# Optimization experiments

Hardware: AMD Instinct MI355X
Metric: run time of the kernel (lower is better)

The kernel has to match this reference:

```python
import jax, jax.numpy as jnp
import numpy as np

D_MODEL = 1024
N_HEADS = 16
HEAD_DIM = D_MODEL // N_HEADS
MAX_LEN = 32768
Q_LEN = 16
START_POS = MAX_LEN - Q_LEN
SCALE = 1.0 / np.sqrt(HEAD_DIM)


def setup_inputs() -> dict:
    key = jax.random.key(0)
    ks = jax.random.split(key, 7)
    xav = np.sqrt(6.0 / (D_MODEL + D_MODEL))  # xavier_uniform bound
    return {
        "query": jax.random.normal(ks[0], (Q_LEN, D_MODEL), dtype=jnp.float32),
        "Wq": jax.random.uniform(ks[1], (D_MODEL, D_MODEL), jnp.float32, -xav, xav),
        "Wk": jax.random.uniform(ks[2], (D_MODEL, D_MODEL), jnp.float32, -xav, xav),
        "Wv": jax.random.uniform(ks[3], (D_MODEL, D_MODEL), jnp.float32, -xav, xav),
        "Wo": jax.random.uniform(ks[4], (D_MODEL, D_MODEL), jnp.float32, -xav, xav),
        "cache_k": jax.random.normal(ks[5], (MAX_LEN, N_HEADS, HEAD_DIM), dtype=jnp.float32),
        "cache_v": jax.random.normal(ks[6], (MAX_LEN, N_HEADS, HEAD_DIM), dtype=jnp.float32),
        "start_pos": START_POS,
    }


def reference(query, Wq, Wk, Wv, Wo, cache_k, cache_v, start_pos):
    S = query.shape[0]
    # QKV projections (nn.Linear: y = x @ W.T), reshape to [S, H, hd]
    Q = (query @ Wq.T).reshape(S, N_HEADS, HEAD_DIM)
    K = (query @ Wk.T).reshape(S, N_HEADS, HEAD_DIM)
    V = (query @ Wv.T).reshape(S, N_HEADS, HEAD_DIM)
    # KV-cache update: write new K/V at start_pos, attend over [0, start_pos+S)
    T = start_pos + S  # cached_seq_len (static python int)
    cached_K = jax.lax.dynamic_update_slice(cache_k, K, (start_pos, 0, 0))[:T]
    cached_V = jax.lax.dynamic_update_slice(cache_v, V, (start_pos, 0, 0))[:T]
    # scores: [H, S, T]
    scores = jnp.einsum("shd,thd->hst", Q, cached_K) * jnp.float32(SCALE)
    if T > S:
        # mask key pos j > query row i + start_pos (triu with diagonal=start_pos+1)
        row = jnp.arange(S)[:, None]
        col = jnp.arange(T)[None, :]
        scores = jnp.where(col > row + start_pos, jnp.float32(-jnp.inf), scores)
    attn = jax.nn.softmax(scores, axis=-1)
    out = jnp.einsum("hst,thd->shd", attn, cached_V).reshape(S, D_MODEL)
    output = out @ Wo.T
    return output, K, V
```

## Files before the change

kernel.cpp:

```cpp
#include <hip/hip_runtime.h>

#define D      1024
#define H      16
#define HD     64
#define SQ     16
#define SP     32752
#define TT     32768
#define SCALE  0.125f
#define NC     64
#define CHUNK  512
#define PSTR   516

__device__ __forceinline__ float4 ldg4(const float* p){ return *reinterpret_cast<const float4*>(p); }
__device__ __forceinline__ void   stg4(float* p, float4 v){ *reinterpret_cast<float4*>(p) = v; }

__device__ __forceinline__ float gemm16_val(const float* __restrict__ x,
                                            const float* __restrict__ W,
                                            int ochunk, int* o_out, int* li_out)
{
    const int t  = threadIdx.x;
    const int o  = ochunk * 16 + (t >> 4);
    const int ds = (t & 15) << 6;

    float4 wv[16];
    const float* wp = W + (size_t)o * D + ds;
    #pragma unroll
    for (int d4 = 0; d4 < 16; ++d4) wv[d4] = ldg4(wp + d4 * 4);

    float a[16];
    #pragma unroll
    for (int i = 0; i < 16; ++i) {
        const float* xp = x + (size_t)i * D + ds;
        float s = 0.f;
        #pragma unroll
        for (int d4 = 0; d4 < 16; ++d4) {
            float4 xv = ldg4(xp + d4 * 4);
            s += wv[d4].x * xv.x + wv[d4].y * xv.y + wv[d4].z * xv.z + wv[d4].w * xv.w;
        }
        a[i] = s;
    }
    #pragma unroll
    for (int off = 8; off >= 1; off >>= 1) {
        #pragma unroll
        for (int i = 0; i < 16; ++i) a[i] += __shfl_xor(a[i], off, 16);
    }
    const int li = t & 15;
    float v = a[0];
    #pragma unroll
    for (int i = 1; i < 16; ++i) v = (li == i) ? a[i] : v;
    *o_out = o; *li_out = li;
    return v;
}

__global__ __launch_bounds__(256) void qkv_proj(
    const float* __restrict__ q,
    const float* __restrict__ Wq, const float* __restrict__ Wk, const float* __restrict__ Wv,
    float* __restrict__ Qws, float* __restrict__ out,
    float* __restrict__ ck, float* __restrict__ cv)
{
    const int m      = blockIdx.x >> 6;
    const int ochunk = blockIdx.x & 63;
    const float* W = (m == 0) ? Wq : (m == 1) ? Wk : Wv;
    int o, li;
    float v = gemm16_val(q, W, ochunk, &o, &li);
    if (m == 0) {
        Qws[li * D + o] = v;
    } else if (m == 1) {
        out[16384 + li * D + o] = v;
        ck[(size_t)(SP + li) * D + o] = v;
    } else {
        out[32768 + li * D + o] = v;
        cv[(size_t)(SP + li) * D + o] = v;
    }
}

__global__ __launch_bounds__(256) void out_proj(
    const float* __restrict__ O, const float* __restrict__ Wo, float* __restrict__ out)
{
    int o, li;
    float v = gemm16_val(O, Wo, blockIdx.x, &o, &li);
    out[li * D + o] = v;
}

__global__ __launch_bounds__(256) void attn_partial(
    const float* __restrict__ Qws, const float* __restrict__ K, const float* __restrict__ V,
    float* __restrict__ num, float* __restrict__ den)
{
    __shared__ float4 q_s[256];
    __shared__ __align__(16) float p_s[16 * PSTR];

    const int t     = threadIdx.x;
    const int h     = blockIdx.x & 15;
    const int c     = blockIdx.x >> 4;
    const int cbase = c * CHUNK;

    {
        const int i = t >> 4, d4 = t & 15;
        q_s[t] = ldg4(Qws + (size_t)i * D + h * HD + d4 * 4);
    }
    __syncthreads();

    {
        const int w  = t >> 6, l = t & 63;
        const int jj = w * 128 + l * 2;
        const int j0 = cbase + jj;
        const float* k0 = K + (size_t)j0 * D + h * HD;
        const float* k1 = k0 + D;

        float s0[16], s1[16];
        #pragma unroll
        for (int i = 0; i < 16; ++i) { s0[i] = 0.f; s1[i] = 0.f; }

        #pragma unroll
        for (int d4 = 0; d4 < 16; ++d4) {
            float4 ka = ldg4(k0 + d4 * 4);
            float4 kb = ldg4(k1 + d4 * 4);
            #pragma unroll
            for (int i = 0; i < 16; ++i) {
                float4 qv = q_s[i * 16 + d4];
                s0[i] += ka.x * qv.x + ka.y * qv.y + ka.z * qv.z + ka.w * qv.w;
                s1[i] += kb.x * qv.x + kb.y * qv.y + kb.z * qv.z + kb.w * qv.w;
            }
        }
        if (j0 >= SP) {
            #pragma unroll
            for (int i = 0; i < 16; ++i) {
                float p0 = (j0     <= SP + i) ? __expf(s0[i] * SCALE) : 0.f;
                float p1 = (j0 + 1 <= SP + i) ? __expf(s1[i] * SCALE) : 0.f;
                *reinterpret_cast<float2*>(&p_s[i * PSTR + jj]) = make_float2(p0, p1);
            }
        } else {
            #pragma unroll
            for (int i = 0; i < 16; ++i) {
                float p0 = __expf(s0[i] * SCALE);
                float p1 = __expf(s1[i] * SCALE);
                *reinterpret_cast<float2*>(&p_s[i * PSTR + jj]) = make_float2(p0, p1);
            }
        }
    }
    __syncthreads();

    {
        const int i = t >> 4, d4 = t & 15;
        const float* vp = V + (size_t)cbase * D + h * HD + d4 * 4;
        const float* pr = p_s + i * PSTR;
        float4 oacc = make_float4(0.f, 0.f, 0.f, 0.f);
        float  dsum = 0.f;
        #pragma unroll 4
        for (int j = 0; j < CHUNK; j += 4) {
            float4 p4 = *reinterpret_cast<const float4*>(pr + j);
            float4 v0 = ldg4(vp + (size_t)(j + 0) * D);
            float4 v1 = ldg4(vp + (size_t)(j + 1) * D);
            float4 v2 = ldg4(vp + (size_t)(j + 2) * D);
            float4 v3 = ldg4(vp + (size_t)(j + 3) * D);
            oacc.x += p4.x * v0.x + p4.y * v1.x + p4.z * v2.x + p4.w * v3.x;
            oacc.y += p4.x * v0.y + p4.y * v1.y + p4.z * v2.y + p4.w * v3.y;
            oacc.z += p4.x * v0.z + p4.y * v1.z + p4.z * v2.z + p4.w * v3.z;
            oacc.w += p4.x * v0.w + p4.y * v1.w + p4.z * v2.w + p4.w * v3.w;
            dsum   += p4.x + p4.y + p4.z + p4.w;
        }
        float* np = num + ((size_t)(h * NC + c) * 16 + i) * 64 + d4 * 4;
        stg4(np, oacc);
        if (d4 == 0) den[(h * NC + c) * 16 + i] = dsum;
    }
}

__global__ __launch_bounds__(256) void combine(
    const float* __restrict__ num, const float* __restrict__ den, float* __restrict__ O)
{
    const int idx = blockIdx.x * 256 + threadIdx.x;
    const int d  = idx & 63;
    const int hh = (idx >> 6) & 15;
    const int i  = idx >> 10;
    float ns = 0.f, ds = 0.f;
    #pragma unroll 8
    for (int c = 0; c < NC; ++c) {
        ns += num[((size_t)(hh * NC + c) * 16 + i) * 64 + d];
        ds += den[(hh * NC + c) * 16 + i];
    }
    O[idx] = ns / ds;
}

extern "C" void kernel_launch(void* const* d_in, const int* in_sizes, int n_in,
                              void* d_out, int out_size, void* d_ws, size_t ws_size,
                              hipStream_t stream)
{
    (void)in_sizes; (void)n_in; (void)out_size; (void)ws_size;
    const float* q  = (const float*)d_in[0];
    const float* Wq = (const float*)d_in[1];
    const float* Wk = (const float*)d_in[2];
    const float* Wv = (const float*)d_in[3];
    const float* Wo = (const float*)d_in[4];
    float* ck  = (float*)d_in[5];
    float* cv  = (float*)d_in[6];
    float* out = (float*)d_out;

    float* ws  = (float*)d_ws;
    float* Qws = ws;
    float* num = ws + 16384;
    float* den = num + (size_t)16 * NC * 16 * 64;
    float* O   = den + 16 * NC * 16;

    qkv_proj   <<<192,     256, 0, stream>>>(q, Wq, Wk, Wv, Qws, out, ck, cv);
    attn_partial<<<16 * NC, 256, 0, stream>>>(Qws, ck, cv, num, den);
    combine    <<<64,      256, 0, stream>>>(num, den, O);
    out_proj   <<<64,      256, 0, stream>>>(O, Wo, out);
}
```

Before: 423.7 us.

## Double attention chunks, split PV across j-subgroups, keep new K/V in workspace

Halves the chunk size to 256 keys so twice as many blocks (2048) cover the cache. Each thread now computes one score per key, and the P·V stage splits keys four ways across thread groups, with each thread accumulating four query rows before a shared-memory reduction. New K/V rows go to a workspace buffer instead of the input cache tensors, and the attention kernel reads from that buffer for the last 16 positions. This aims to raise parallelism and reuse of V loads, at the cost of more partials for the combine step and extra shared-memory traffic.

Result: faster. 387.9 us (-8.5%).

```diff
diff --git a/kernel.cpp b/kernel.cpp
--- a/kernel.cpp
+++ b/kernel.cpp
@@ -3,13 +3,12 @@
 #define D      1024
 #define H      16
 #define HD     64
-#define SQ     16
 #define SP     32752
 #define TT     32768
 #define SCALE  0.125f
-#define NC     64
-#define CHUNK  512
-#define PSTR   516
+#define NC     128
+#define CHUNK  256
+#define PSTR   260
 
 __device__ __forceinline__ float4 ldg4(const float* p){ return *reinterpret_cast<const float4*>(p); }
 __device__ __forceinline__ void   stg4(float* p, float4 v){ *reinterpret_cast<float4*>(p) = v; }
@@ -56,7 +55,7 @@
     const float* __restrict__ q,
     const float* __restrict__ Wq, const float* __restrict__ Wk, const float* __restrict__ Wv,
     float* __restrict__ Qws, float* __restrict__ out,
-    float* __restrict__ ck, float* __restrict__ cv)
+    float* __restrict__ Kn, float* __restrict__ Vn)
 {
     const int m      = blockIdx.x >> 6;
     const int ochunk = blockIdx.x & 63;
@@ -67,10 +66,10 @@
         Qws[li * D + o] = v;
     } else if (m == 1) {
         out[16384 + li * D + o] = v;
-        ck[(size_t)(SP + li) * D + o] = v;
+        Kn[li * D + o] = v;
     } else {
         out[32768 + li * D + o] = v;
-        cv[(size_t)(SP + li) * D + o] = v;
+        Vn[li * D + o] = v;
     }
 }
 
@@ -84,10 +83,12 @@
 
 __global__ __launch_bounds__(256) void attn_partial(
     const float* __restrict__ Qws, const float* __restrict__ K, const float* __restrict__ V,
+    const float* __restrict__ Kn, const float* __restrict__ Vn,
     float* __restrict__ num, float* __restrict__ den)
 {
     __shared__ float4 q_s[256];
     __shared__ __align__(16) float p_s[16 * PSTR];
+    __shared__ float den_s[64];
 
     const int t     = threadIdx.x;
     const int h     = blockIdx.x & 15;
@@ -101,67 +102,123 @@
     __syncthreads();
 
     {
-        const int w  = t >> 6, l = t & 63;
-        const int jj = w * 128 + l * 2;
-        const int j0 = cbase + jj;
-        const float* k0 = K + (size_t)j0 * D + h * HD;
-        const float* k1 = k0 + D;
-
-        float s0[16], s1[16];
-        #pragma unroll
-        for (int i = 0; i < 16; ++i) { s0[i] = 0.f; s1[i] = 0.f; }
-
+        const int j0 = cbase + t;
+        const float* kp = (j0 < SP) ? (K  + (size_t)j0        * D + h * HD)
+                                    : (Kn + (size_t)(j0 - SP) * D + h * HD);
+        float s[16];
+        #pragma unroll
+        for (int i = 0; i < 16; ++i) s[i] = 0.f;
         #pragma unroll
         for (int d4 = 0; d4 < 16; ++d4) {
-            float4 ka = ldg4(k0 + d4 * 4);
-            float4 kb = ldg4(k1 + d4 * 4);
+            float4 kv = ldg4(kp + d4 * 4);
             #pragma unroll
             for (int i = 0; i < 16; ++i) {
                 float4 qv = q_s[i * 16 + d4];
-                s0[i] += ka.x * qv.x + ka.y * qv.y + ka.z * qv.z + ka.w * qv.w;
-                s1[i] += kb.x * qv.x + kb.y * qv.y + kb.z * qv.z + kb.w * qv.w;
+                s[i] += kv.x * qv.x + kv.y * qv.y + kv.z * qv.z + kv.w * qv.w;
             }
         }
         if (j0 >= SP) {
             #pragma unroll
-            for (int i = 0; i < 16; ++i) {
-                float p0 = (j0     <= SP + i) ? __expf(s0[i] * SCALE) : 0.f;
-                float p1 = (j0 + 1 <= SP + i) ? __expf(s1[i] * SCALE) : 0.f;
-                *reinterpret_cast<float2*>(&p_s[i * PSTR + jj]) = make_float2(p0, p1);
+            for (int i = 0; i < 16; ++i)
+                p_s[i * PSTR + t] = (j0 <= SP + i) ? __expf(s[i] * SCALE) : 0.f;
+        } else {
+            #pragma unroll
+            for (int i = 0; i < 16; ++i)
+                p_s[i * PSTR + t] = __expf(s[i] * SCALE);
+        }
+    }
+    __syncthreads();
+
+    const int d4 = t & 15, ig = (t >> 4) & 3, jsub = t >> 6;
+    float4 a0 = make_float4(0.f,0.f,0.f,0.f), a1 = a0, a2 = a0, a3 = a0;
+    float  e0 = 0.f, e1 = 0.f, e2 = 0.f, e3 = 0.f;
+    {
+        const int jb = jsub * 64;
+        const float* vp  = V + (size_t)(cbase + jb) * D + h * HD + d4 * 4;
+        const float* p0r = p_s + (4 * ig + 0) * PSTR + jb;
+        const float* p1r = p0r + PSTR;
+        const float* p2r = p1r + PSTR;
+        const float* p3r = p2r + PSTR;
+        if (!(c == NC - 1 && jsub == 3)) {
+            #pragma unroll 2
+            for (int j = 0; j < 64; j += 4) {
+                float4 pA = *reinterpret_cast<const float4*>(p0r + j);
+                float4 pB = *reinterpret_cast<const float4*>(p1r + j);
+                float4 pC = *reinterpret_cast<const float4*>(p2r + j);
+                float4 pD = *reinterpret_cast<const float4*>(p3r + j);
+                float4 v0 = ldg4(vp + (size_t)(j + 0) * D);
+                float4 v1 = ldg4(vp + (size_t)(j + 1) * D);
+                float4 v2 = ldg4(vp + (size_t)(j + 2) * D);
+                float4 v3 = ldg4(vp + (size_t)(j + 3) * D);
+                a0.x += pA.x*v0.x + pA.y*v1.x + pA.z*v2.x + pA.w*v3.x;
+                a0.y += pA.x*v0.y + pA.y*v1.y + pA.z*v2.y + pA.w*v3.y;
+                a0.z += pA.x*v0.z + pA.y*v1.z + pA.z*v2.z + pA.w*v3.z;
+                a0.w += pA.x*v0.w + pA.y*v1.w + pA.z*v2.w + pA.w*v3.w;
+                a1.x += pB.x*v0.x + pB.y*v1.x + pB.z*v2.x + pB.w*v3.x;
+                a1.y += pB.x*v0.y + pB.y*v1.y + pB.z*v2.y + pB.w*v3.y;
+                a1.z += pB.x*v0.z + pB.y*v1.z + pB.z*v2.z + pB.w*v3.z;
+                a1.w += pB.x*v0.w + pB.y*v1.w + pB.z*v2.w + pB.w*v3.w;
+                a2.x += pC.x*v0.x + pC.y*v1.x + pC.z*v2.x + pC.w*v3.x;
+                a2.y += pC.x*v0.y + pC.y*v1.y + pC.z*v2.y + pC.w*v3.y;
+                a2.z += pC.x*v0.z + pC.y*v1.z + pC.z*v2.z + pC.w*v3.z;
+                a2.w += pC.x*v0.w + pC.y*v1.w + pC.z*v2.w + pC.w*v3.w;
+                a3.x += pD.x*v0.x + pD.y*v1.x + pD.z*v2.x + pD.w*v3.x;
+                a3.y += pD.x*v0.y + pD.y*v1.y + pD.z*v2.y + pD.w*v3.y;
+                a3.z += pD.x*v0.z + pD.y*v1.z + pD.z*v2.z + pD.w*v3.z;
+                a3.w += pD.x*v0.w + pD.y*v1.w + pD.z*v2.w + pD.w*v3.w;
+                e0 += (pA.x + pA.y) + (pA.z + pA.w);
+                e1 += (pB.x + pB.y) + (pB.z + pB.w);
+                e2 += (pC.x + pC.y) + (pC.z + pC.w);
+                e3 += (pD.x + pD.y) + (pD.z + pD.w);
             }
         } else {
-            #pragma unroll
-            for (int i = 0; i < 16; ++i) {
-                float p0 = __expf(s0[i] * SCALE);
-                float p1 = __expf(s1[i] * SCALE);
-                *reinterpret_cast<float2*>(&p_s[i * PSTR + jj]) = make_float2(p0, p1);
+            for (int j = 0; j < 64; ++j) {
+                const int jg = cbase + jb + j;
+                const float* vr = (jg < SP) ? (vp + (size_t)j * D)
+                                            : (Vn + (size_t)(jg - SP) * D + h * HD + d4 * 4);
+                float4 vv = ldg4(vr);
+                float pa = p0r[j], pb = p1r[j], pc = p2r[j], pd = p3r[j];
+                a0.x += pa*vv.x; a0.y += pa*vv.y; a0.z += pa*vv.z; a0.w += pa*vv.w;
+                a1.x += pb*vv.x; a1.y += pb*vv.y; a1.z += pb*vv.z; a1.w += pb*vv.w;
+                a2.x += pc*vv.x; a2.y += pc*vv.y; a2.z += pc*vv.z; a2.w += pc*vv.w;
+                a3.x += pd*vv.x; a3.y += pd*vv.y; a3.z += pd*vv.z; a3.w += pd*vv.w;
+                e0 += pa; e1 += pb; e2 += pc; e3 += pd;
             }
         }
     }
     __syncthreads();
 
     {
-        const int i = t >> 4, d4 = t & 15;
-        const float* vp = V + (size_t)cbase * D + h * HD + d4 * 4;
-        const float* pr = p_s + i * PSTR;
-        float4 oacc = make_float4(0.f, 0.f, 0.f, 0.f);
-        float  dsum = 0.f;
-        #pragma unroll 4
-        for (int j = 0; j < CHUNK; j += 4) {
-            float4 p4 = *reinterpret_cast<const float4*>(pr + j);
-            float4 v0 = ldg4(vp + (size_t)(j + 0) * D);
-            float4 v1 = ldg4(vp + (size_t)(j + 1) * D);
-            float4 v2 = ldg4(vp + (size_t)(j + 2) * D);
-            float4 v3 = ldg4(vp + (size_t)(j + 3) * D);
-            oacc.x += p4.x * v0.x + p4.y * v1.x + p4.z * v2.x + p4.w * v3.x;
-            oacc.y += p4.x * v0.y + p4.y * v1.y + p4.z * v2.y + p4.w * v3.y;
-            oacc.z += p4.x * v0.z + p4.y * v1.z + p4.z * v2.z + p4.w * v3.z;
-            oacc.w += p4.x * v0.w + p4.y * v1.w + p4.z * v2.w + p4.w * v3.w;
-            dsum   += p4.x + p4.y + p4.z + p4.w;
-        }
-        float* np = num + ((size_t)(h * NC + c) * 16 + i) * 64 + d4 * 4;
-        stg4(np, oacc);
-        if (d4 == 0) den[(h * NC + c) * 16 + i] = dsum;
+        float* ob = p_s + jsub * 1024 + (ig * 16 + d4) * 16;
+        stg4(ob + 0,  a0);
+        stg4(ob + 4,  a1);
+        stg4(ob + 8,  a2);
+        stg4(ob + 12, a3);
+        if (d4 == 0) {
+            den_s[jsub * 16 + ig * 4 + 0] = e0;
+            den_s[jsub * 16 + ig * 4 + 1] = e1;
+            den_s[jsub * 16 + ig * 4 + 2] = e2;
+            den_s[jsub * 16 + ig * 4 + 3] = e3;
+        }
+    }
+    __syncthreads();
+
+    {
+        const int i = t >> 4, dq = t & 15;
+        const int off = ((i >> 2) * 16 + dq) * 16 + (i & 3) * 4;
+        float4 r0 = *reinterpret_cast<const float4*>(p_s + off);
+        float4 r1 = *reinterpret_cast<const float4*>(p_s + 1024 + off);
+        float4 r2 = *reinterpret_cast<const float4*>(p_s + 2048 + off);
+        float4 r3 = *reinterpret_cast<const float4*>(p_s + 3072 + off);
+        float4 o;
+        o.x = (r0.x + r1.x) + (r2.x + r3.x);
+        o.y = (r0.y + r1.y) + (r2.y + r3.y);
+        o.z = (r0.z + r1.z) + (r2.z + r3.z);
+        o.w = (r0.w + r1.w) + (r2.w + r3.w);
+        stg4(num + ((size_t)(h * NC + c) * 16 + i) * 64 + dq * 4, o);
+        if (t < 16)
+            den[(h * NC + c) * 16 + t] =
+                (den_s[t] + den_s[16 + t]) + (den_s[32 + t] + den_s[48 + t]);
     }
 }
 
@@ -191,18 +248,20 @@
     const float* Wk = (const float*)d_in[2];
     const float* Wv = (const float*)d_in[3];
     const float* Wo = (const float*)d_in[4];
-    float* ck  = (float*)d_in[5];
-    float* cv  = (float*)d_in[6];
+    const float* ck = (const float*)d_in[5];
+    const float* cv = (const float*)d_in[6];
     float* out = (float*)d_out;
 
     float* ws  = (float*)d_ws;
     float* Qws = ws;
-    float* num = ws + 16384;
+    float* Kn  = ws + 16384;
+    float* Vn  = ws + 32768;
+    float* num = ws + 49152;
     float* den = num + (size_t)16 * NC * 16 * 64;
-    float* O   = den + 16 * NC * 16;
-
-    qkv_proj   <<<192,     256, 0, stream>>>(q, Wq, Wk, Wv, Qws, out, ck, cv);
-    attn_partial<<<16 * NC, 256, 0, stream>>>(Qws, ck, cv, num, den);
-    combine    <<<64,      256, 0, stream>>>(num, den, O);
-    out_proj   <<<64,      256, 0, stream>>>(O, Wo, out);
-}
+    float* O   = den + (size_t)16 * NC * 16;
+
+    qkv_proj    <<<192,     256, 0, stream>>>(q, Wq, Wk, Wv, Qws, out, Kn, Vn);
+    attn_partial<<<16 * NC, 256, 0, stream>>>(Qws, ck, cv, Kn, Vn, num, den);
+    combine     <<<64,      256, 0, stream>>>(num, den, O);
+    out_proj    <<<64,      256, 0, stream>>>(O, Wo, out);
+}
```
